# Kernel tuning notes

Hardware: AMD Instinct MI355X
Metric: run time of the kernel (lower is better)

The kernel has to match this reference:

```python
import jax, jax.numpy as jnp
import numpy as np
import math

SZ = 1024
N = 65536  # number of rows (tokens) in x


def setup_inputs() -> dict:
    key = jax.random.key(0)
    kx, kA = jax.random.split(key)
    x = jax.random.normal(kx, (N, SZ), dtype=jnp.float32)
    A = jax.random.normal(kA, (SZ, SZ), dtype=jnp.float32) * math.sqrt(2.0 / SZ)
    b = jnp.zeros((SZ,), dtype=jnp.float32)
    return {"x": x, "A": A, "b": b}


def _precalc(A):
    # B = A A^T; sequential triangular elimination on p (faithful to torch loop):
    # for i in range(sz-1): p[i+1:] -= (2*B[i, i+1:] / diag[i+1:])[:, None] * p[i]
    sz = A.shape[0]
    B = A @ A.T                       # [sz, sz]
    diag = jnp.diagonal(B)            # [sz]
    rows = jnp.arange(sz)

    def step(p, i):
        coef = 2.0 * B[i] / diag      # [sz]; only entries j > i are applied
        coef = jnp.where(rows > i, coef, 0.0)
        p = p - coef[:, None] * p[i]  # rank-1 update of rows below i
        return p, None

    p, _ = jax.lax.scan(step, A, jnp.arange(sz - 1))
    return p, diag


def reference(x, A, b):
    p, diag = _precalc(A)
    Bx = x @ A.T                      # [N, sz]
    out = x - (2.0 * Bx / diag) @ p   # [N, sz]
    return out + b
```

## Files before the change

kernel.cpp:

```cpp
#include <hip/hip_runtime.h>
#include <hip/hip_bf16.h>

typedef unsigned short u16;
typedef float f32x4 __attribute__((ext_vector_type(4)));
typedef u16   u16x8 __attribute__((ext_vector_type(8)));
typedef u16   u16x4 __attribute__((ext_vector_type(4)));
typedef short s16x8 __attribute__((ext_vector_type(8)));

__device__ __forceinline__ u16 f2bf(float f) {
  unsigned u = __builtin_bit_cast(unsigned, f);
  unsigned r = (u + 0x7fffu + ((u >> 16) & 1u)) >> 16;
  return (u16)r;
}
__device__ __forceinline__ u16 cvtbf(float f) {
  return __builtin_bit_cast(u16, __float2bfloat16(f));
}

#define GL_LDS16(gp, lp)                                                     \
  __builtin_amdgcn_global_load_lds((const __attribute__((address_space(1))) void*)(gp), \
                                   (__attribute__((address_space(3))) void*)(lp), 16, 0, 0)

__global__ __launch_bounds__(256) void k_bbtx(const float* __restrict__ A, float* __restrict__ B,
                                              float* __restrict__ rd2,
                                              const float* __restrict__ X, u16* __restrict__ Xbf) {
  const int bid = blockIdx.x;
  const int tid = threadIdx.x;
  if (bid >= 256) {
    const int vb = bid - 256;
    for (int gid = vb * 256 + tid; gid < (1 << 23); gid += 2048 * 256) {
      const int mi   = gid >> 15;
      const int it   = (gid >> 11) & 15;
      const int kt2  = (gid >> 10) & 1;
      const int msub = (gid >> 6) & 15;
      const int lane = gid & 63;
      const int m = mi * 256 + msub * 16 + (lane & 15);
      const int k = it * 64 + kt2 * 32 + (lane >> 4) * 8;
      const float* s = X + (size_t)m * 1024 + k;
      f32x4 u = *(const f32x4*)s;
      f32x4 v = *(const f32x4*)(s + 4);
      u16x8 h;
      h[0] = cvtbf(u[0]); h[1] = cvtbf(u[1]); h[2] = cvtbf(u[2]); h[3] = cvtbf(u[3]);
      h[4] = cvtbf(v[0]); h[5] = cvtbf(v[1]); h[6] = cvtbf(v[2]); h[7] = cvtbf(v[3]);
      *(u16x8*)(Xbf + (size_t)gid * 8) = h;
    }
    return;
  }
  __shared__ float s0[32][68];
  __shared__ float s1[32][68];
  const int i0 = (bid >> 4) * 64, j0 = (bid & 15) * 64;
  const int tx = tid & 15, ty = tid >> 4;
  const int sr = tid >> 2, sc = (tid & 3) * 8;
  f32x4 acc[4];
#pragma unroll
  for (int q = 0; q < 4; ++q) acc[q] = {0.f, 0.f, 0.f, 0.f};

  for (int k0 = 0; k0 < 1024; k0 += 32) {
    f32x4 a0 = *(const f32x4*)&A[(size_t)(i0 + sr) * 1024 + k0 + sc];
    f32x4 a1 = *(const f32x4*)&A[(size_t)(i0 + sr) * 1024 + k0 + sc + 4];
    f32x4 b0 = *(const f32x4*)&A[(size_t)(j0 + sr) * 1024 + k0 + sc];
    f32x4 b1 = *(const f32x4*)&A[(size_t)(j0 + sr) * 1024 + k0 + sc + 4];
    __syncthreads();
#pragma unroll
    for (int q = 0; q < 4; ++q) {
      s0[sc + q][sr] = a0[q]; s0[sc + 4 + q][sr] = a1[q];
      s1[sc + q][sr] = b0[q]; s1[sc + 4 + q][sr] = b1[q];
    }
    __syncthreads();
#pragma unroll
    for (int kk = 0; kk < 32; ++kk) {
      f32x4 av = *(const f32x4*)&s0[kk][ty * 4];
      f32x4 bv = *(const f32x4*)&s1[kk][tx * 4];
#pragma unroll
      for (int q = 0; q < 4; ++q) acc[q] += bv * av[q];
    }
  }
#pragma unroll
  for (int q = 0; q < 4; ++q)
    *(f32x4*)&B[(size_t)(i0 + ty * 4 + q) * 1024 + j0 + tx * 4] = acc[q];
  if (i0 == j0 && tx == ty) {
#pragma unroll
    for (int q = 0; q < 4; ++q) rd2[i0 + ty * 4 + q] = 2.0f / acc[q][q];
  }
}

__global__ __launch_bounds__(256) void k_tinv(const float* __restrict__ B, const float* __restrict__ rd2,
                                              float* __restrict__ M) {
  __shared__ float Ct[64][68];
  __shared__ float rdl[64];
  const int tid = threadIdx.x;
  const int k0 = blockIdx.x * 64;
  if (tid < 64) rdl[tid] = rd2[k0 + tid];
  __syncthreads();
  {
    const int i = tid >> 2, j0q = (tid & 3) * 16;
#pragma unroll
    for (int jj = 0; jj < 16; ++jj) {
      int j = j0q + jj;
      Ct[i][j] = (j > i) ? B[(size_t)(k0 + i) * 1024 + k0 + j] * rdl[j] : 0.0f;
    }
  }
  __syncthreads();
  if (tid < 64) {
    float pc[64];
#pragma unroll
    for (int r = 0; r < 64; ++r) pc[r] = (r == tid) ? 1.0f : 0.0f;
#pragma unroll
    for (int i = 0; i < 63; ++i) {
      const float pi = pc[i];
#pragma unroll
      for (int j = i + 1; j < 64; ++j) pc[j] -= Ct[i][j] * pi;
    }
#pragma unroll
    for (int r = 0; r < 64; ++r) M[(size_t)(k0 + r) * 1024 + k0 + tid] = pc[r];
  }
}

__global__ __launch_bounds__(256) void k_u(const float* __restrict__ B, const float* __restrict__ rd2,
                                           const float* __restrict__ M, float* __restrict__ U, int lvl) {
  __shared__ float sA[32][68];
  __shared__ float sB[32][68];
  const int tid = threadIdx.x;
  const int s = 64 << lvl;
  const int ti = blockIdx.x >> lvl, tj = blockIdx.x & ((1 << lvl) - 1);
  const int a = blockIdx.y * (s << 1);
  const int m0 = a + s + ti * 64;
  const int n0 = a + tj * 64;
  const int tx = tid & 15, ty = tid >> 4;
  const int asr = tid >> 2, asc = (tid & 3) * 8;
  const int bkr = tid >> 3, bnc = (tid & 7) * 8;
  const float r2 = rd2[m0 + asr];
  f32x4 acc[4];
#pragma unroll
  for (int q = 0; q < 4; ++q) acc[q] = {0.f, 0.f, 0.f, 0.f};

  for (int k0 = 0; k0 < s; k0 += 32) {
    f32x4 a0 = *(const f32x4*)&B[(size_t)(m0 + asr) * 1024 + a + k0 + asc];
    f32x4 a1 = *(const f32x4*)&B[(size_t)(m0 + asr) * 1024 + a + k0 + asc + 4];
    f32x4 b0 = *(const f32x4*)&M[(size_t)(a + k0 + bkr) * 1024 + n0 + bnc];
    f32x4 b1 = *(const f32x4*)&M[(size_t)(a + k0 + bkr) * 1024 + n0 + bnc + 4];
    a0 *= r2; a1 *= r2;
    __syncthreads();
#pragma unroll
    for (int q = 0; q < 4; ++q) { sA[asc + q][asr] = a0[q]; sA[asc + 4 + q][asr] = a1[q]; }
    *(f32x4*)&sB[bkr][bnc] = b0;
    *(f32x4*)&sB[bkr][bnc + 4] = b1;
    __syncthreads();
#pragma unroll
    for (int kk = 0; kk < 32; ++kk) {
      f32x4 av = *(const f32x4*)&sA[kk][ty * 4];
      f32x4 bv = *(const f32x4*)&sB[kk][tx * 4];
#pragma unroll
      for (int q = 0; q < 4; ++q) acc[q] += bv * av[q];
    }
  }
  float* up = U + (size_t)blockIdx.y * s * s;
#pragma unroll
  for (int q = 0; q < 4; ++q)
    *(f32x4*)&up[(size_t)(ti * 64 + ty * 4 + q) * s + tj * 64 + tx * 4] = acc[q];
}

__global__ __launch_bounds__(256) void k_moff(float* __restrict__ M, const float* __restrict__ U, int lvl) {
  __shared__ float sA[32][68];
  __shared__ float sB[32][68];
  const int tid = threadIdx.x;
  const int s = 64 << lvl;
  const int ti = blockIdx.x >> lvl, tj = blockIdx.x & ((1 << lvl) - 1);
  const int a = blockIdx.y * (s << 1);
  const int m0 = a + s + ti * 64;
  const int n0 = a + tj * 64;
  const int tx = tid & 15, ty = tid >> 4;
  const int asr = tid >> 2, asc = (tid & 3) * 8;
  const int bkr = tid >> 3, bnc = (tid & 7) * 8;
  const float* up = U + (size_t)blockIdx.y * s * s;
  f32x4 acc[4];
#pragma unroll
  for (int q = 0; q < 4; ++q) acc[q] = {0.f, 0.f, 0.f, 0.f};

  for (int k0 = 0; k0 < s; k0 += 32) {
    f32x4 a0 = *(const f32x4*)&M[(size_t)(m0 + asr) * 1024 + a + s + k0 + asc];
    f32x4 a1 = *(const f32x4*)&M[(size_t)(m0 + asr) * 1024 + a + s + k0 + asc + 4];
    f32x4 b0 = *(const f32x4*)&up[(size_t)(k0 + bkr) * s + tj * 64 + bnc];
    f32x4 b1 = *(const f32x4*)&up[(size_t)(k0 + bkr) * s + tj * 64 + bnc + 4];
    __syncthreads();
#pragma unroll
    for (int q = 0; q < 4; ++q) { sA[asc + q][asr] = a0[q]; sA[asc + 4 + q][asr] = a1[q]; }
    *(f32x4*)&sB[bkr][bnc] = b0;
    *(f32x4*)&sB[bkr][bnc + 4] = b1;
    __syncthreads();
#pragma unroll
    for (int kk = 0; kk < 32; ++kk) {
      f32x4 av = *(const f32x4*)&sA[kk][ty * 4];
      f32x4 bv = *(const f32x4*)&sB[kk][tx * 4];
#pragma unroll
      for (int q = 0; q < 4; ++q) acc[q] += bv * av[q];
    }
  }
#pragma unroll
  for (int q = 0; q < 4; ++q)
    *(f32x4*)&M[(size_t)(m0 + ty * 4 + q) * 1024 + n0 + tx * 4] = -acc[q];
}

__global__ __launch_bounds__(256) void k_yma(const float* __restrict__ M, const float* __restrict__ A,
                                             float* __restrict__ Y) {
  __shared__ float sA[32][68];
  __shared__ float sB[32][68];
  const int tid = threadIdx.x;
  const int ri = blockIdx.y, cj = blockIdx.x;
  const int m0 = ri * 64, n0 = cj * 64;
  const int kmax = (ri + 1) * 64;
  const int tx = tid & 15, ty = tid >> 4;
  const int asr = tid >> 2, asc = (tid & 3) * 8;
  const int bkr = tid >> 3, bnc = (tid & 7) * 8;
  f32x4 acc[4];
#pragma unroll
  for (int q = 0; q < 4; ++q) acc[q] = {0.f, 0.f, 0.f, 0.f};

  for (int k0 = 0; k0 < kmax; k0 += 32) {
    f32x4 a0 = *(const f32x4*)&M[(size_t)(m0 + asr) * 1024 + k0 + asc];
    f32x4 a1 = *(const f32x4*)&M[(size_t)(m0 + asr) * 1024 + k0 + asc + 4];
    f32x4 b0 = *(const f32x4*)&A[(size_t)(k0 + bkr) * 1024 + n0 + bnc];
    f32x4 b1 = *(const f32x4*)&A[(size_t)(k0 + bkr) * 1024 + n0 + bnc + 4];
    __syncthreads();
#pragma unroll
    for (int q = 0; q < 4; ++q) { sA[asc + q][asr] = a0[q]; sA[asc + 4 + q][asr] = a1[q]; }
    *(f32x4*)&sB[bkr][bnc] = b0;
    *(f32x4*)&sB[bkr][bnc + 4] = b1;
    __syncthreads();
#pragma unroll
    for (int kk = 0; kk < 32; ++kk) {
      f32x4 av = *(const f32x4*)&sA[kk][ty * 4];
      f32x4 bv = *(const f32x4*)&sB[kk][tx * 4];
#pragma unroll
      for (int q = 0; q < 4; ++q) acc[q] += bv * av[q];
    }
  }
#pragma unroll
  for (int q = 0; q < 4; ++q)
    *(f32x4*)&Y[(size_t)(m0 + ty * 4 + q) * 1024 + n0 + tx * 4] = acc[q];
}

__global__ __launch_bounds__(256) void k_w(const float* __restrict__ A, const float* __restrict__ P,
                                           const float* __restrict__ rd2, u16* __restrict__ Wf) {
  __shared__ float As[32][68];
  __shared__ float Ps[32][68];
  const int tid = threadIdx.x;
  const int kb = blockIdx.y * 64, nb = blockIdx.x * 64;
  const int sr = tid >> 3, sc = (tid & 7) * 8;
  const int tx = tid & 15, ty = tid >> 4;
  f32x4 acc[4];
#pragma unroll
  for (int q = 0; q < 4; ++q) acc[q] = {0.f, 0.f, 0.f, 0.f};

  for (int i0 = 0; i0 < 1024; i0 += 32) {
    float r2 = rd2[i0 + sr];
    f32x4 a0 = *(const f32x4*)&A[(size_t)(i0 + sr) * 1024 + kb + sc];
    f32x4 a1 = *(const f32x4*)&A[(size_t)(i0 + sr) * 1024 + kb + sc + 4];
    f32x4 p0 = *(const f32x4*)&P[(size_t)(i0 + sr) * 1024 + nb + sc];
    f32x4 p1 = *(const f32x4*)&P[(size_t)(i0 + sr) * 1024 + nb + sc + 4];
    __syncthreads();
    *(f32x4*)&As[sr][sc]     = a0 * r2;
    *(f32x4*)&As[sr][sc + 4] = a1 * r2;
    *(f32x4*)&Ps[sr][sc]     = p0;
    *(f32x4*)&Ps[sr][sc + 4] = p1;
    __syncthreads();
#pragma unroll
    for (int i = 0; i < 32; ++i) {
      f32x4 av = *(const f32x4*)&As[i][ty * 4];
      f32x4 pv = *(const f32x4*)&Ps[i][tx * 4];
#pragma unroll
      for (int q = 0; q < 4; ++q) acc[q] += pv * av[q];
    }
  }
  const int ktile = (kb + ty * 4) >> 5;
  const int kg = ((ty * 4) >> 3) & 3;
  const int e0 = (ty * 4) & 7;
#pragma unroll
  for (int j = 0; j < 4; ++j) {
    int n = nb + tx * 4 + j;
    int nt = n >> 4;
    int ln = kg * 16 + (n & 15);
    u16x4 pk;
#pragma unroll
    for (int q = 0; q < 4; ++q) {
      int kk = kb + ty * 4 + q;
      float w = ((kk == n) ? 1.0f : 0.0f) - acc[q][j];
      pk[q] = f2bf(w);
    }
    *(u16x4*)&Wf[((size_t)(ktile * 64 + nt) * 64 + ln) * 8 + e0] = pk;
  }
}

template<int I>
__device__ __forceinline__ void phase_body(const u16* __restrict__ ax, const u16* __restrict__ wbase,
                                           u16* As, u16* Bs, int tid, int wr, int wc, int lane,
                                           f32x4 (&acc)[8][4],
                                           s16x8 (&afA)[8], s16x8 (&bfA)[4],
                                           s16x8 (&afB)[8], s16x8 (&bfB)[4]) {
  s16x8 (&afC)[8] = ((I & 1) == 0) ? afA : afB;
  s16x8 (&bfC)[4] = ((I & 1) == 0) ? bfA : bfB;
  s16x8 (&afN)[8] = ((I & 1) == 0) ? afB : afA;
  s16x8 (&bfN)[4] = ((I & 1) == 0) ? bfB : bfA;

  if constexpr (I <= 29)      asm volatile("s_waitcnt vmcnt(4)" ::: "memory");
  else if constexpr (I == 30) asm volatile("s_waitcnt vmcnt(0)" ::: "memory");
  if constexpr (I <= 30) __builtin_amdgcn_s_barrier();

  if constexpr (I + 3 < 32) {
    constexpr int j = I + 3, jt = j >> 1, jk = j & 1, js = j & 3;
    GL_LDS16(ax + (size_t)jt * 16384 + jk * 8192 + tid * 8,            As + js * 8192 + tid * 8);
    GL_LDS16(ax + (size_t)jt * 16384 + jk * 8192 + 4096 + tid * 8,     As + js * 8192 + 4096 + tid * 8);
    GL_LDS16(wbase + (size_t)jt * 65536 + jk * 32768 + tid * 8,        Bs + js * 8192 + tid * 8);
    GL_LDS16(wbase + (size_t)jt * 65536 + jk * 32768 + 4096 + tid * 8, Bs + js * 8192 + 4096 + tid * 8);
  }
  if constexpr (I + 1 < 32) {
    constexpr int js = (I + 1) & 3;
    const u16* Asb = As + js * 8192;
    const u16* Bsb = Bs + js * 8192;
#pragma unroll
    for (int m = 0; m < 8; ++m) afN[m] = *(const s16x8*)&Asb[(wr * 8 + m) * 512 + lane * 8];
#pragma unroll
    for (int n = 0; n < 4; ++n) bfN[n] = *(const s16x8*)&Bsb[(wc * 4 + n) * 512 + lane * 8];
  }
  __builtin_amdgcn_s_setprio(1);
#pragma unroll
  for (int m = 0; m < 8; ++m)
#pragma unroll
    for (int n = 0; n < 4; ++n)
      acc[m][n] = __builtin_amdgcn_mfma_f32_16x16x32_bf16(afC[m], bfC[n], acc[m][n], 0, 0, 0);
  __builtin_amdgcn_s_setprio(0);
}

__global__ __launch_bounds__(512, 2) void k_out8(const u16* __restrict__ Xbf, const u16* __restrict__ Wf,
                                                 const float* __restrict__ bvec, float* __restrict__ out) {
  __shared__ u16 As[32768];
  __shared__ u16 Bs[32768];
  const int tid = threadIdx.x;
  const int lane = tid & 63, wid = tid >> 6;
  const int wr = wid >> 2, wc = wid & 3;
  const int lin = blockIdx.x;
  const int xcd = lin & 7, idx = lin >> 3;
  const int mi = xcd * 32 + (idx >> 2);
  const int ni = idx & 3;

  const u16* ax = Xbf + (size_t)mi * 262144;
  const u16* wbase = Wf + (size_t)ni * 8192;

  f32x4 acc[8][4];
#pragma unroll
  for (int m = 0; m < 8; ++m)
#pragma unroll
    for (int n = 0; n < 4; ++n) acc[m][n] = {0.f, 0.f, 0.f, 0.f};

#pragma unroll
  for (int j = 0; j < 3; ++j) {
    const int jt = j >> 1, jk = j & 1;
    GL_LDS16(ax + (size_t)jt * 16384 + jk * 8192 + tid * 8,            As + j * 8192 + tid * 8);
    GL_LDS16(ax + (size_t)jt * 16384 + jk * 8192 + 4096 + tid * 8,     As + j * 8192 + 4096 + tid * 8);
    GL_LDS16(wbase + (size_t)jt * 65536 + jk * 32768 + tid * 8,        Bs + j * 8192 + tid * 8);
    GL_LDS16(wbase + (size_t)jt * 65536 + jk * 32768 + 4096 + tid * 8, Bs + j * 8192 + 4096 + tid * 8);
  }
  asm volatile("s_waitcnt vmcnt(8)" ::: "memory");
  __builtin_amdgcn_s_barrier();

  s16x8 afA[8], bfA[4], afB[8], bfB[4];
#pragma unroll
  for (int m = 0; m < 8; ++m) afA[m] = *(const s16x8*)&As[(wr * 8 + m) * 512 + lane * 8];
#pragma unroll
  for (int n = 0; n < 4; ++n) bfA[n] = *(const s16x8*)&Bs[(wc * 4 + n) * 512 + lane * 8];

#define PH(I) phase_body<I>(ax, wbase, As, Bs, tid, wr, wc, lane, acc, afA, bfA, afB, bfB);
  PH(0)  PH(1)  PH(2)  PH(3)  PH(4)  PH(5)  PH(6)  PH(7)
  PH(8)  PH(9)  PH(10) PH(11) PH(12) PH(13) PH(14) PH(15)
  PH(16) PH(17) PH(18) PH(19) PH(20) PH(21) PH(22) PH(23)
  PH(24) PH(25) PH(26) PH(27) PH(28) PH(29) PH(30) PH(31)
#undef PH

  const long orow0 = (long)mi * 256 + wr * 128 + (lane >> 4) * 4;
  const int  ocol0 = ni * 256 + wc * 64 + (lane & 15);
#pragma unroll
  for (int aj = 0; aj < 4; ++aj) {
    const int cc = ocol0 + aj * 16;
    const float bb = bvec[cc];
#pragma unroll
    for (int ai = 0; ai < 8; ++ai) {
      const long r = orow0 + ai * 16;
#pragma unroll
      for (int q = 0; q < 4; ++q)
        out[(r + q) * 1024 + cc] = acc[ai][aj][q] + bb;
    }
  }
}

__global__ __launch_bounds__(256) void k_out_r(const float* __restrict__ X, const u16* __restrict__ Wf,
                                               const float* __restrict__ bvec, float* __restrict__ out) {
  __shared__ u16 As[8192];
  __shared__ u16 Bs[8192];
  const int tid = threadIdx.x;
  const int lane = tid & 63, wid = tid >> 6;
  const int wr = wid >> 1, wc = wid & 1;
  const int lin = blockIdx.x;
  const int mi = (lin & 7) * 64 + (lin >> 6);
  const int ni = (lin >> 3) & 7;
  const long m0 = (long)mi * 128;
  const int n0 = ni * 128;

  const float *xs0, *xs1, *xs2, *xs3;
  int aw0, aw1, aw2, aw3;
#define APREP(J, XS, AW) { int c = (J) * 256 + tid; int m = c >> 3, kg8 = c & 7;       \
    XS = X + (m0 + m) * 1024 + kg8 * 8;                                                \
    int kt2 = kg8 >> 2, ks = kg8 & 3, msub = m >> 4, mm = m & 15;                      \
    AW = (((kt2 * 8 + msub) * 64 + ks * 16 + mm) * 16) ^ (ks << 4); }
  APREP(0, xs0, aw0) APREP(1, xs1, aw1) APREP(2, xs2, aw2) APREP(3, xs3, aw3)
#undef APREP

  const u16* wsrc0 = Wf + (size_t)ni * 4096 + tid * 8;
  u16* bd0 = Bs + tid * 8;
  const int aro = (lane * 16) ^ (((lane >> 4) & 3) << 4);
  const char* Ab = (const char*)As + aro;
  const char* Bb = (const char*)Bs + lane * 16;

  f32x4 acc[4][4];
#pragma unroll
  for (int m = 0; m < 4; ++m)
#pragma unroll
    for (int n = 0; n < 4; ++n) acc[m][n] = {0.f, 0.f, 0.f, 0.f};

  for (int it = 0; it < 16; ++it) {
    const u16* w0 = wsrc0 + (size_t)it * 65536;
    GL_LDS16(w0,          bd0);
    GL_LDS16(w0 + 2048,   bd0 + 2048);
    GL_LDS16(w0 + 32768,  bd0 + 4096);
    GL_LDS16(w0 + 34816,  bd0 + 6144);
    const int ko = it * 64;
#define ASTAGE(XS, AW) { f32x4 u = *(const f32x4*)((XS) + ko); f32x4 v = *(const f32x4*)((XS) + ko + 4); \
    u16x8 h;                                                                              \
    h[0] = cvtbf(u[0]); h[1] = cvtbf(u[1]); h[2] = cvtbf(u[2]); h[3] = cvtbf(u[3]);       \
    h[4] = cvtbf(v[0]); h[5] = cvtbf(v[1]); h[6] = cvtbf(v[2]); h[7] = cvtbf(v[3]);       \
    *(u16x8*)((char*)As + (AW)) = h; }
    ASTAGE(xs0, aw0) ASTAGE(xs1, aw1) ASTAGE(xs2, aw2) ASTAGE(xs3, aw3)
#undef ASTAGE
    __syncthreads();
#pragma unroll
    for (int kt2 = 0; kt2 < 2; ++kt2) {
      s16x8 af[4], bfr[4];
#pragma unroll
      for (int m = 0; m < 4; ++m) af[m] = *(const s16x8*)(Ab + ((kt2 * 8 + wr * 4 + m) << 10));
#pragma unroll
      for (int n = 0; n < 4; ++n) bfr[n] = *(const s16x8*)(Bb + ((kt2 * 8 + wc * 4 + n) << 10));
#pragma unroll
      for (int m = 0; m < 4; ++m)
#pragma unroll
        for (int n = 0; n < 4; ++n)
          acc[m][n] = __builtin_amdgcn_mfma_f32_16x16x32_bf16(af[m], bfr[n], acc[m][n], 0, 0, 0);
    }
    __syncthreads();
  }

  const long orow0 = m0 + wr * 64 + (lane >> 4) * 4;
  const int  ocol0 = n0 + wc * 64 + (lane & 15);
#pragma unroll
  for (int n = 0; n < 4; ++n) {
    const int cc = ocol0 + n * 16;
    const float bb = bvec[cc];
#pragma unroll
    for (int m = 0; m < 4; ++m) {
      const long r = orow0 + m * 16;
#pragma unroll
      for (int q = 0; q < 4; ++q)
        out[(r + q) * 1024 + cc] = acc[m][n][q] + bb;
    }
  }
}

extern "C" void kernel_launch(void* const* d_in, const int* in_sizes, int n_in,
                              void* d_out, int out_size, void* d_ws, size_t ws_size,
                              hipStream_t stream) {
  const float* x  = (const float*)d_in[0];
  const float* A  = (const float*)d_in[1];
  const float* bv = (const float*)d_in[2];
  float* out = (float*)d_out;
  char* ws = (char*)d_ws;

  float* B   = (float*)(ws);
  float* Y   = B;
  float* M   = (float*)(ws + (4u << 20));
  u16*   Wf  = (u16*)  (ws + (8u << 20));
  float* rd2 = (float*)(ws + (10u << 20));
  float* U   = (float*)(ws + (10u << 20) + 65536);
  u16*   Xbf = (u16*)  (ws + (12u << 20));

  const size_t need = (12u << 20) + (size_t)65536 * 1024 * 2;
  const bool big = (ws_size >= need);

  hipMemsetAsync(M, 0, 1024 * 1024 * sizeof(float), stream);
  k_bbtx<<<big ? 2304 : 256, 256, 0, stream>>>(A, B, rd2, x, Xbf);
  k_tinv<<<16, 256, 0, stream>>>(B, rd2, M);
  for (int lvl = 0; lvl < 4; ++lvl) {
    const int nt2 = 1 << (2 * lvl);
    const int np  = 8 >> lvl;
    k_u<<<dim3(nt2, np), 256, 0, stream>>>(B, rd2, M, U, lvl);
    k_moff<<<dim3(nt2, np), 256, 0, stream>>>(M, U, lvl);
  }
  k_yma<<<dim3(16, 16), 256, 0, stream>>>(M, A, Y);
  k_w<<<dim3(16, 16), 256, 0, stream>>>(A, Y, rd2, Wf);

  if (big) {
    k_out8<<<1024, 512, 0, stream>>>(Xbf, Wf, bv, out);
  } else {
    k_out_r<<<4096, 256, 0, stream>>>(x, Wf, bv, out);
  }
}
```

Before: 564.5 us.

## Exploit symmetry and triangularity in precalc, stream W fragments directly from global

Computes only the upper-triangular tiles of A·A^T and mirrors them into the lower half. Fuses the first doubling level of the triangular inverse into one kernel. Bounds the k-loops in k_u and k_moff so they skip known-zero triangular blocks, and drops the memset of M. In the main bf16 GEMM, W fragments are now loaded straight from global memory into registers instead of staging through LDS, which frees LDS and allows a deeper A prefetch. The risks are extra global-load latency on the W operand and any reader of M that relies on its upper triangle having been zeroed.

```diff
diff --git a/kernel.cpp b/kernel.cpp
--- a/kernel.cpp
+++ b/kernel.cpp
@@ -25,9 +25,8 @@
                                               const float* __restrict__ X, u16* __restrict__ Xbf) {
   const int bid = blockIdx.x;
   const int tid = threadIdx.x;
-  if (bid >= 256) {
-    const int vb = bid - 256;
-    for (int gid = vb * 256 + tid; gid < (1 << 23); gid += 2048 * 256) {
+  if (bid >= 136) {
+    for (int gid = (bid - 136) * 256 + tid; gid < (1 << 23); gid += 2048 * 256) {
       const int mi   = gid >> 15;
       const int it   = (gid >> 11) & 15;
       const int kt2  = (gid >> 10) & 1;
@@ -47,7 +46,10 @@
   }
   __shared__ float s0[32][68];
   __shared__ float s1[32][68];
-  const int i0 = (bid >> 4) * 64, j0 = (bid & 15) * 64;
+  int t = bid, ii = 0;
+  while (t >= 16 - ii) { t -= 16 - ii; ++ii; }
+  const int jj = ii + t;
+  const int i0 = ii * 64, j0 = jj * 64;
   const int tx = tid & 15, ty = tid >> 4;
   const int sr = tid >> 2, sc = (tid & 3) * 8;
   f32x4 acc[4];
@@ -77,7 +79,13 @@
 #pragma unroll
   for (int q = 0; q < 4; ++q)
     *(f32x4*)&B[(size_t)(i0 + ty * 4 + q) * 1024 + j0 + tx * 4] = acc[q];
-  if (i0 == j0 && tx == ty) {
+  if (ii != jj) {
+#pragma unroll
+    for (int q = 0; q < 4; ++q)
+#pragma unroll
+      for (int w = 0; w < 4; ++w)
+        B[(size_t)(j0 + tx * 4 + w) * 1024 + i0 + ty * 4 + q] = acc[q][w];
+  } else if (tx == ty) {
 #pragma unroll
     for (int q = 0; q < 4; ++q) rd2[i0 + ty * 4 + q] = 2.0f / acc[q][q];
   }
@@ -113,6 +121,65 @@
 #pragma unroll
     for (int r = 0; r < 64; ++r) M[(size_t)(k0 + r) * 1024 + k0 + tid] = pc[r];
   }
+}
+
+__global__ __launch_bounds__(256) void k_lvl0(const float* __restrict__ B, const float* __restrict__ rd2,
+                                              float* __restrict__ M) {
+  __shared__ float sA[32][68];
+  __shared__ float sB[32][68];
+  __shared__ float Us[64][68];
+  const int tid = threadIdx.x;
+  const int a = blockIdx.x * 128;
+  const int m0 = a + 64;
+  const int tx = tid & 15, ty = tid >> 4;
+  const int asr = tid >> 2, asc = (tid & 3) * 8;
+  const int bkr = tid >> 3, bnc = (tid & 7) * 8;
+  const float r2 = rd2[m0 + asr];
+  f32x4 acc[4];
+#pragma unroll
+  for (int q = 0; q < 4; ++q) acc[q] = {0.f, 0.f, 0.f, 0.f};
+  for (int k0 = 0; k0 < 64; k0 += 32) {
+    f32x4 a0 = *(const f32x4*)&B[(size_t)(m0 + asr) * 1024 + a + k0 + asc];
+    f32x4 a1 = *(const f32x4*)&B[(size_t)(m0 + asr) * 1024 + a + k0 + asc + 4];
+    f32x4 b0 = *(const f32x4*)&M[(size_t)(a + k0 + bkr) * 1024 + a + bnc];
+    f32x4 b1 = *(const f32x4*)&M[(size_t)(a + k0 + bkr) * 1024 + a + bnc + 4];
+    a0 *= r2; a1 *= r2;
+    __syncthreads();
+#pragma unroll
+    for (int q = 0; q < 4; ++q) { sA[asc + q][asr] = a0[q]; sA[asc + 4 + q][asr] = a1[q]; }
+    *(f32x4*)&sB[bkr][bnc] = b0;
+    *(f32x4*)&sB[bkr][bnc + 4] = b1;
+    __syncthreads();
+#pragma unroll
+    for (int kk = 0; kk < 32; ++kk) {
+      f32x4 av = *(const f32x4*)&sA[kk][ty * 4];
+      f32x4 bv = *(const f32x4*)&sB[kk][tx * 4];
+#pragma unroll
+      for (int q = 0; q < 4; ++q) acc[q] += bv * av[q];
+    }
+  }
+#pragma unroll
+  for (int q = 0; q < 4; ++q) *(f32x4*)&Us[ty * 4 + q][tx * 4] = acc[q];
+#pragma unroll
+  for (int q = 0; q < 4; ++q) acc[q] = {0.f, 0.f, 0.f, 0.f};
+  for (int k0 = 0; k0 < 64; k0 += 32) {
+    f32x4 a0 = *(const f32x4*)&M[(size_t)(m0 + asr) * 1024 + m0 + k0 + asc];
+    f32x4 a1 = *(const f32x4*)&M[(size_t)(m0 + asr) * 1024 + m0 + k0 + asc + 4];
+    __syncthreads();
+#pragma unroll
+    for (int q = 0; q < 4; ++q) { sA[asc + q][asr] = a0[q]; sA[asc + 4 + q][asr] = a1[q]; }
+    __syncthreads();
+#pragma unroll
+    for (int kk = 0; kk < 32; ++kk) {
+      f32x4 av = *(const f32x4*)&sA[kk][ty * 4];
+      f32x4 bv = *(const f32x4*)&Us[k0 + kk][tx * 4];
+#pragma unroll
+      for (int q = 0; q < 4; ++q) acc[q] += bv * av[q];
+    }
+  }
+#pragma unroll
+  for (int q = 0; q < 4; ++q)
+    *(f32x4*)&M[(size_t)(m0 + ty * 4 + q) * 1024 + a + tx * 4] = -acc[q];
 }
 
 __global__ __launch_bounds__(256) void k_u(const float* __restrict__ B, const float* __restrict__ rd2,
@@ -133,7 +200,7 @@
 #pragma unroll
   for (int q = 0; q < 4; ++q) acc[q] = {0.f, 0.f, 0.f, 0.f};
 
-  for (int k0 = 0; k0 < s; k0 += 32) {
+  for (int k0 = tj * 64; k0 < s; k0 += 32) {
     f32x4 a0 = *(const f32x4*)&B[(size_t)(m0 + asr) * 1024 + a + k0 + asc];
     f32x4 a1 = *(const f32x4*)&B[(size_t)(m0 + asr) * 1024 + a + k0 + asc + 4];
     f32x4 b0 = *(const f32x4*)&M[(size_t)(a + k0 + bkr) * 1024 + n0 + bnc];
@@ -172,11 +239,12 @@
   const int asr = tid >> 2, asc = (tid & 3) * 8;
   const int bkr = tid >> 3, bnc = (tid & 7) * 8;
   const float* up = U + (size_t)blockIdx.y * s * s;
+  const int kmax = (ti + 1) * 64;
   f32x4 acc[4];
 #pragma unroll
   for (int q = 0; q < 4; ++q) acc[q] = {0.f, 0.f, 0.f, 0.f};
 
-  for (int k0 = 0; k0 < s; k0 += 32) {
+  for (int k0 = 0; k0 < kmax; k0 += 32) {
     f32x4 a0 = *(const f32x4*)&M[(size_t)(m0 + asr) * 1024 + a + s + k0 + asc];
     f32x4 a1 = *(const f32x4*)&M[(size_t)(m0 + asr) * 1024 + a + s + k0 + asc + 4];
     f32x4 b0 = *(const f32x4*)&up[(size_t)(k0 + bkr) * s + tj * 64 + bnc];
@@ -292,7 +360,7 @@
 
 template<int I>
 __device__ __forceinline__ void phase_body(const u16* __restrict__ ax, const u16* __restrict__ wbase,
-                                           u16* As, u16* Bs, int tid, int wr, int wc, int lane,
+                                           u16* As, int tid, int wr, int wc, int lane,
                                            f32x4 (&acc)[8][4],
                                            s16x8 (&afA)[8], s16x8 (&bfA)[4],
                                            s16x8 (&afB)[8], s16x8 (&bfB)[4]) {
@@ -301,25 +369,23 @@
   s16x8 (&afN)[8] = ((I & 1) == 0) ? afB : afA;
   s16x8 (&bfN)[4] = ((I & 1) == 0) ? bfB : bfA;
 
-  if constexpr (I <= 29)      asm volatile("s_waitcnt vmcnt(4)" ::: "memory");
-  else if constexpr (I == 30) asm volatile("s_waitcnt vmcnt(0)" ::: "memory");
-  if constexpr (I <= 30) __builtin_amdgcn_s_barrier();
-
-  if constexpr (I + 3 < 32) {
-    constexpr int j = I + 3, jt = j >> 1, jk = j & 1, js = j & 3;
-    GL_LDS16(ax + (size_t)jt * 16384 + jk * 8192 + tid * 8,            As + js * 8192 + tid * 8);
-    GL_LDS16(ax + (size_t)jt * 16384 + jk * 8192 + 4096 + tid * 8,     As + js * 8192 + 4096 + tid * 8);
-    GL_LDS16(wbase + (size_t)jt * 65536 + jk * 32768 + tid * 8,        Bs + js * 8192 + tid * 8);
-    GL_LDS16(wbase + (size_t)jt * 65536 + jk * 32768 + 4096 + tid * 8, Bs + js * 8192 + 4096 + tid * 8);
+  if constexpr (I <= 30) {
+    asm volatile("s_waitcnt vmcnt(6)" ::: "memory");
+    __builtin_amdgcn_s_barrier();
+  }
+  if constexpr (I + 4 < 32) {
+    constexpr int j = I + 4, jt = j >> 1, jk = j & 1, js = j & 3;
+    GL_LDS16(ax + (size_t)jt * 16384 + jk * 8192 + tid * 8,        As + js * 8192 + tid * 8);
+    GL_LDS16(ax + (size_t)jt * 16384 + jk * 8192 + 4096 + tid * 8, As + js * 8192 + 4096 + tid * 8);
   }
   if constexpr (I + 1 < 32) {
-    constexpr int js = (I + 1) & 3;
+    constexpr int j = I + 1, jt = j >> 1, jk = j & 1, js = j & 3;
+    const u16* bsrc = wbase + (size_t)jt * 65536 + jk * 32768 + wc * 2048 + lane * 8;
+#pragma unroll
+    for (int n = 0; n < 4; ++n) bfN[n] = *(const s16x8*)(bsrc + n * 512);
     const u16* Asb = As + js * 8192;
-    const u16* Bsb = Bs + js * 8192;
 #pragma unroll
     for (int m = 0; m < 8; ++m) afN[m] = *(const s16x8*)&Asb[(wr * 8 + m) * 512 + lane * 8];
-#pragma unroll
-    for (int n = 0; n < 4; ++n) bfN[n] = *(const s16x8*)&Bsb[(wc * 4 + n) * 512 + lane * 8];
   }
   __builtin_amdgcn_s_setprio(1);
 #pragma unroll
@@ -333,7 +399,6 @@
 __global__ __launch_bounds__(512, 2) void k_out8(const u16* __restrict__ Xbf, const u16* __restrict__ Wf,
                                                  const float* __restrict__ bvec, float* __restrict__ out) {
   __shared__ u16 As[32768];
-  __shared__ u16 Bs[32768];
   const int tid = threadIdx.x;
   const int lane = tid & 63, wid = tid >> 6;
   const int wr = wid >> 2, wc = wid & 3;
@@ -352,23 +417,23 @@
     for (int n = 0; n < 4; ++n) acc[m][n] = {0.f, 0.f, 0.f, 0.f};
 
 #pragma unroll
-  for (int j = 0; j < 3; ++j) {
+  for (int j = 0; j < 4; ++j) {
     const int jt = j >> 1, jk = j & 1;
-    GL_LDS16(ax + (size_t)jt * 16384 + jk * 8192 + tid * 8,            As + j * 8192 + tid * 8);
-    GL_LDS16(ax + (size_t)jt * 16384 + jk * 8192 + 4096 + tid * 8,     As + j * 8192 + 4096 + tid * 8);
-    GL_LDS16(wbase + (size_t)jt * 65536 + jk * 32768 + tid * 8,        Bs + j * 8192 + tid * 8);
-    GL_LDS16(wbase + (size_t)jt * 65536 + jk * 32768 + 4096 + tid * 8, Bs + j * 8192 + 4096 + tid * 8);
-  }
-  asm volatile("s_waitcnt vmcnt(8)" ::: "memory");
+    GL_LDS16(ax + (size_t)jt * 16384 + jk * 8192 + tid * 8,        As + j * 8192 + tid * 8);
+    GL_LDS16(ax + (size_t)jt * 16384 + jk * 8192 + 4096 + tid * 8, As + j * 8192 + 4096 + tid * 8);
+  }
+  s16x8 afA[8], bfA[4], afB[8], bfB[4];
+  {
+    const u16* bsrc = wbase + wc * 2048 + lane * 8;
+#pragma unroll
+    for (int n = 0; n < 4; ++n) bfA[n] = *(const s16x8*)(bsrc + n * 512);
+  }
+  asm volatile("s_waitcnt vmcnt(10)" ::: "memory");
   __builtin_amdgcn_s_barrier();
-
-  s16x8 afA[8], bfA[4], afB[8], bfB[4];
 #pragma unroll
   for (int m = 0; m < 8; ++m) afA[m] = *(const s16x8*)&As[(wr * 8 + m) * 512 + lane * 8];
-#pragma unroll
-  for (int n = 0; n < 4; ++n) bfA[n] = *(const s16x8*)&Bs[(wc * 4 + n) * 512 + lane * 8];
-
-#define PH(I) phase_body<I>(ax, wbase, As, Bs, tid, wr, wc, lane, acc, afA, bfA, afB, bfB);
+
+#define PH(I) phase_body<I>(ax, wbase, As, tid, wr, wc, lane, acc, afA, bfA, afB, bfB);
   PH(0)  PH(1)  PH(2)  PH(3)  PH(4)  PH(5)  PH(6)  PH(7)
   PH(8)  PH(9)  PH(10) PH(11) PH(12) PH(13) PH(14) PH(15)
   PH(16) PH(17) PH(18) PH(19) PH(20) PH(21) PH(22) PH(23)
@@ -492,10 +557,10 @@
   const size_t need = (12u << 20) + (size_t)65536 * 1024 * 2;
   const bool big = (ws_size >= need);
 
-  hipMemsetAsync(M, 0, 1024 * 1024 * sizeof(float), stream);
-  k_bbtx<<<big ? 2304 : 256, 256, 0, stream>>>(A, B, rd2, x, Xbf);
+  k_bbtx<<<big ? 2184 : 136, 256, 0, stream>>>(A, B, rd2, x, Xbf);
   k_tinv<<<16, 256, 0, stream>>>(B, rd2, M);
-  for (int lvl = 0; lvl < 4; ++lvl) {
+  k_lvl0<<<8, 256, 0, stream>>>(B, rd2, M);
+  for (int lvl = 1; lvl < 4; ++lvl) {
     const int nt2 = 1 << (2 * lvl);
     const int np  = 8 >> lvl;
     k_u<<<dim3(nt2, np), 256, 0, stream>>>(B, rd2, M, U, lvl);
```

Result: slower. 598.0 us (+5.9%).
